# Kernel optimization log

Measured on AMD Instinct MI355X. Metric: run time of the kernel, lower is better.

The kernel has to match this reference:

```python
import jax, jax.numpy as jnp
import numpy as np

S = 100   # n_pred_samples
B = 64    # batch
DIMS = [784, 512, 512, 10]


def setup_inputs() -> dict:
    key = jax.random.key(0)
    ks = jax.random.split(key, 16)
    d = {}
    d["inputs"] = jax.random.normal(ks[0], (B, DIMS[0]), dtype=jnp.float32)
    d["task_id"] = 0
    # variational params: means ~ 0.1*N(0,1), logvars constant -6 (as in module init)
    d["wm0"] = jax.random.normal(ks[1], (DIMS[0], DIMS[1])) * 0.1
    d["wv0"] = jnp.full((DIMS[0], DIMS[1]), -6.0, jnp.float32)
    d["bm0"] = jnp.full((DIMS[1],), 0.1, jnp.float32)
    d["bv0"] = jnp.full((DIMS[1],), -6.0, jnp.float32)
    d["wm1"] = jax.random.normal(ks[2], (DIMS[1], DIMS[2])) * 0.1
    d["wv1"] = jnp.full((DIMS[1], DIMS[2]), -6.0, jnp.float32)
    d["bm1"] = jnp.full((DIMS[2],), 0.1, jnp.float32)
    d["bv1"] = jnp.full((DIMS[2],), -6.0, jnp.float32)
    d["wml"] = jax.random.normal(ks[3], (DIMS[2], DIMS[3])) * 0.1
    d["wvl"] = jnp.full((DIMS[2], DIMS[3]), -6.0, jnp.float32)
    d["bml"] = jnp.full((DIMS[3],), 0.1, jnp.float32)
    d["bvl"] = jnp.full((DIMS[3],), -6.0, jnp.float32)
    # reparameterization noise (passed explicitly for determinism)
    d["we0"] = jax.random.normal(ks[4], (S, DIMS[0], DIMS[1]), dtype=jnp.float32)
    d["be0"] = jax.random.normal(ks[5], (S, 1, DIMS[1]), dtype=jnp.float32)
    d["we1"] = jax.random.normal(ks[6], (S, DIMS[1], DIMS[2]), dtype=jnp.float32)
    d["be1"] = jax.random.normal(ks[7], (S, 1, DIMS[2]), dtype=jnp.float32)
    d["wel"] = jax.random.normal(ks[8], (S, DIMS[2], DIMS[3]), dtype=jnp.float32)
    d["bel"] = jax.random.normal(ks[9], (S, 1, DIMS[3]), dtype=jnp.float32)
    return d


def _sample(eps, logvar, mean):
    # reparameterization: eps * exp(0.5*logvar) + mean
    return eps * jnp.exp(0.5 * logvar) + mean


def reference(inputs, task_id, wm0, wv0, bm0, bv0, wm1, wv1, bm1, bv1,
              wml, wvl, bml, bvl, we0, be0, we1, be1, wel, bel):
    # activations: [S, B, D]
    act = jnp.broadcast_to(inputs[None], (S,) + inputs.shape)
    # hidden layer 0
    W0 = _sample(we0, wv0, wm0)          # [S, D0, D1]
    b0 = _sample(be0, bv0, bm0)          # [S, 1, D1]
    act = jax.nn.relu(jnp.einsum('sbi,sio->sbo', act, W0) + b0)
    # hidden layer 1
    W1 = _sample(we1, wv1, wm1)
    b1 = _sample(be1, bv1, bm1)
    act = jax.nn.relu(jnp.einsum('sbi,sio->sbo', act, W1) + b1)
    # last (task-specific) layer: original does broadcast-mul + sum over dim 2,
    # which is exactly a batched matmul — expressed here as an einsum
    Wl = _sample(wel, wvl, wml)          # [S, D2, O]
    bl = _sample(bel, bvl, bml)          # [S, 1, O]
    logits = jnp.einsum('sbh,sho->sbo', act, Wl) + bl   # [S, B, O]
    return logits
```

## Files before the change

### kernel.cpp

```cpp
#include <hip/hip_runtime.h>
#include <hip/hip_bf16.h>


typedef __bf16 bf16x8 __attribute__((ext_vector_type(8)));
typedef float f32x4 __attribute__((ext_vector_type(4)));

#define NSAMP 100
#define BATCH 64
#define D0 784
#define D1 512
#define D2 512
#define DOUT 10
#define K0PAD 800
#define RSB 40

__device__ __forceinline__ unsigned short f2bf(float f) {
    __bf16 b = (__bf16)f;
    return __builtin_bit_cast(unsigned short, b);
}
__device__ __forceinline__ float bf_hi(unsigned int u) {
    return __builtin_bit_cast(float, u & 0xffff0000u);
}
__device__ __forceinline__ float bf_lo(unsigned int u) {
    return __builtin_bit_cast(float, u << 16);
}

union FragU { uint4 q; bf16x8 v; };

#define XB_N   (BATCH * K0PAD)
#define PS0_N  (D0 * D1)
#define PS1_N  (D1 * D2)
#define SGL_N  (D2 * DOUT)
#define B0_N   (NSAMP * D1)
#define B1_N   (NSAMP * D2)
#define BL_N   (NSAMP * DOUT)
#define PREP_TOTAL (XB_N + PS0_N + PS1_N + SGL_N + B0_N + B1_N + BL_N)

__global__ __launch_bounds__(256) void prep(
    const float* __restrict__ inputs,
    const float* __restrict__ wv0, const float* __restrict__ wm0,
    const float* __restrict__ wv1, const float* __restrict__ wm1,
    const float* __restrict__ wvl,
    const float* __restrict__ be0, const float* __restrict__ bv0, const float* __restrict__ bm0,
    const float* __restrict__ be1, const float* __restrict__ bv1, const float* __restrict__ bm1,
    const float* __restrict__ bel, const float* __restrict__ bvl, const float* __restrict__ bml,
    unsigned short* __restrict__ Xb,
    unsigned int* __restrict__ psm0, unsigned int* __restrict__ psm1,
    float* __restrict__ sigmal,
    float* __restrict__ bias0, float* __restrict__ bias1, float* __restrict__ biasl)
{
    int i = blockIdx.x * 256 + threadIdx.x;
    if (i < XB_N) {
        int m = i / K0PAD, k = i % K0PAD;
        float v = (k < D0) ? inputs[m * D0 + k] : 0.f;
        Xb[i] = f2bf(v);
        return;
    }
    i -= XB_N;
    if (i < PS0_N) {
        unsigned int sg = f2bf(__expf(0.5f * wv0[i]));
        unsigned int mn = f2bf(wm0[i]);
        psm0[i] = (sg << 16) | mn;
        return;
    }
    i -= PS0_N;
    if (i < PS1_N) {
        unsigned int sg = f2bf(__expf(0.5f * wv1[i]));
        unsigned int mn = f2bf(wm1[i]);
        psm1[i] = (sg << 16) | mn;
        return;
    }
    i -= PS1_N;
    if (i < SGL_N) { sigmal[i] = __expf(0.5f * wvl[i]); return; }
    i -= SGL_N;
    if (i < B0_N) { int n = i % D1; bias0[i] = fmaf(be0[i], __expf(0.5f * bv0[n]), bm0[n]); return; }
    i -= B0_N;
    if (i < B1_N) { int n = i % D2; bias1[i] = fmaf(be1[i], __expf(0.5f * bv1[n]), bm1[n]); return; }
    i -= B1_N;
    if (i < BL_N) { int o = i % DOUT; biasl[i] = fmaf(bel[i], __expf(0.5f * bvl[o]), bml[o]); return; }
}

__global__ __launch_bounds__(64) void gemm_wave(
    const unsigned short* __restrict__ A, int lda, long aStride,
    const float* __restrict__ eps, long eStride,
    const unsigned int* __restrict__ psm,
    int KT, int Kvalid,
    const float* __restrict__ bias,
    void* __restrict__ outp, int outBf16)
{
    __shared__ unsigned short smB[32 * RSB];

    const int bx = blockIdx.x;
    const int s  = bx >> 4;
    const int n0 = (bx & 15) << 5;
    const int l  = threadIdx.x;
    const int fr = l & 15, quad = l >> 4;
    const int kg = l >> 3;
    const int ng = l & 7;

    const unsigned short* aP = A + (long)s * aStride + (long)fr * lda + quad * 8;
    const float* eB        = eps + (long)s * eStride + n0 + 4 * ng;
    const unsigned int* pB = psm + n0 + 4 * ng;

    f32x4 acc[4][2] = {};

    float4 ea0[4], ea1[4];
    uint4  pa0[4], pa1[4], aa0[4], aa1[4];

    auto loadAll = [&](int kt, float4* ea, uint4* pa, uint4* aa) {
        const int kb = kt * 32;
#pragma unroll
        for (int mi = 0; mi < 4; ++mi)
            aa[mi] = *reinterpret_cast<const uint4*>(aP + (long)(mi * 16) * lda + kb);
#pragma unroll
        for (int j = 0; j < 4; ++j) {
            const int row = kb + 4 * kg + j;
            const bool ok = row < Kvalid;
            const long off = (long)(ok ? row : 0) * 512;
            float4 e = *reinterpret_cast<const float4*>(eB + off);
            uint4  p = *reinterpret_cast<const uint4*>(pB + off);
            if (!ok) { e = float4{0.f, 0.f, 0.f, 0.f}; p = uint4{0u, 0u, 0u, 0u}; }
            ea[j] = e; pa[j] = p;
        }
    };

    auto stage = [&](const float4* ea, const uint4* pa) {
        float w[4][4];
#pragma unroll
        for (int j = 0; j < 4; ++j) {
            w[j][0] = fmaf(ea[j].x, bf_hi(pa[j].x), bf_lo(pa[j].x));
            w[j][1] = fmaf(ea[j].y, bf_hi(pa[j].y), bf_lo(pa[j].y));
            w[j][2] = fmaf(ea[j].z, bf_hi(pa[j].z), bf_lo(pa[j].z));
            w[j][3] = fmaf(ea[j].w, bf_hi(pa[j].w), bf_lo(pa[j].w));
        }
#pragma unroll
        for (int i = 0; i < 4; ++i) {
            uint2 d;
            d.x = (unsigned)f2bf(w[0][i]) | ((unsigned)f2bf(w[1][i]) << 16);
            d.y = (unsigned)f2bf(w[2][i]) | ((unsigned)f2bf(w[3][i]) << 16);
            *reinterpret_cast<uint2*>(&smB[(4 * ng + i) * RSB + 4 * kg]) = d;
        }
    };

    auto compute = [&](const uint4* aa) {
        FragU bf0, bf1;
        bf0.q = *reinterpret_cast<const uint4*>(&smB[fr * RSB + quad * 8]);
        bf1.q = *reinterpret_cast<const uint4*>(&smB[(16 + fr) * RSB + quad * 8]);
#pragma unroll
        for (int mi = 0; mi < 4; ++mi) {
            FragU af; af.q = aa[mi];
            acc[mi][0] = __builtin_amdgcn_mfma_f32_16x16x32_bf16(af.v, bf0.v, acc[mi][0], 0, 0, 0);
            acc[mi][1] = __builtin_amdgcn_mfma_f32_16x16x32_bf16(af.v, bf1.v, acc[mi][1], 0, 0, 0);
        }
    };

    loadAll(0, ea0, pa0, aa0);
    int kt = 0;
    for (; kt + 2 <= KT; kt += 2) {
        loadAll(kt + 1, ea1, pa1, aa1);
        stage(ea0, pa0);
        compute(aa0);
        if (kt + 2 < KT) loadAll(kt + 2, ea0, pa0, aa0);
        stage(ea1, pa1);
        compute(aa1);
    }
    if (kt < KT) { stage(ea0, pa0); compute(aa0); }

    const float bv0v = bias[(long)s * 512 + n0 + fr];
    const float bv1v = bias[(long)s * 512 + n0 + 16 + fr];
    const long outBase = (long)s * BATCH * 512;
#pragma unroll
    for (int mi = 0; mi < 4; ++mi) {
#pragma unroll
        for (int ni = 0; ni < 2; ++ni) {
            const float bv = ni ? bv1v : bv0v;
            const int col = n0 + ni * 16 + fr;
#pragma unroll
            for (int r = 0; r < 4; ++r) {
                const int row = mi * 16 + quad * 4 + r;
                float v = fmaxf(acc[mi][ni][r] + bv, 0.f);
                const long idx = outBase + (long)row * 512 + col;
                if (outBf16) ((unsigned short*)outp)[idx] = f2bf(v);
                else         ((float*)outp)[idx] = v;
            }
        }
    }
}

__global__ __launch_bounds__(320) void last_layer(
    const float* __restrict__ act2,
    const float* __restrict__ wel,
    const float* __restrict__ sigmal,
    const float* __restrict__ wml,
    const float* __restrict__ biasl,
    float* __restrict__ out)
{
    __shared__ float smW[D2 * DOUT];
    const int s = blockIdx.x;
    const int t = threadIdx.x;
    const float* we = wel + (long)s * D2 * DOUT;
    for (int i = t; i < D2 * DOUT; i += 320)
        smW[i] = fmaf(we[i], sigmal[i], wml[i]);
    __syncthreads();

    const int m  = t / 5;
    const int op = t % 5;
    const float* a = act2 + ((long)s * BATCH + m) * D2;
    float acc0 = 0.f, acc1 = 0.f;
#pragma unroll 4
    for (int k = 0; k < D2; k += 4) {
        float4 av = *reinterpret_cast<const float4*>(a + k);
        acc0 = fmaf(av.x, smW[(k + 0) * DOUT + op], acc0);
        acc0 = fmaf(av.y, smW[(k + 1) * DOUT + op], acc0);
        acc0 = fmaf(av.z, smW[(k + 2) * DOUT + op], acc0);
        acc0 = fmaf(av.w, smW[(k + 3) * DOUT + op], acc0);
        acc1 = fmaf(av.x, smW[(k + 0) * DOUT + op + 5], acc1);
        acc1 = fmaf(av.y, smW[(k + 1) * DOUT + op + 5], acc1);
        acc1 = fmaf(av.z, smW[(k + 2) * DOUT + op + 5], acc1);
        acc1 = fmaf(av.w, smW[(k + 3) * DOUT + op + 5], acc1);
    }
    const long ob = ((long)s * BATCH + m) * DOUT;
    out[ob + op]     = acc0 + biasl[s * DOUT + op];
    out[ob + op + 5] = acc1 + biasl[s * DOUT + op + 5];
}

extern "C" void kernel_launch(void* const* d_in, const int* in_sizes, int n_in,
                              void* d_out, int out_size, void* d_ws, size_t ws_size,
                              hipStream_t stream)
{
    const float* inputs = (const float*)d_in[0];
    const float* wm0 = (const float*)d_in[2];
    const float* wv0 = (const float*)d_in[3];
    const float* bm0 = (const float*)d_in[4];
    const float* bv0 = (const float*)d_in[5];
    const float* wm1 = (const float*)d_in[6];
    const float* wv1 = (const float*)d_in[7];
    const float* bm1 = (const float*)d_in[8];
    const float* bv1 = (const float*)d_in[9];
    const float* wml = (const float*)d_in[10];
    const float* wvl = (const float*)d_in[11];
    const float* bml = (const float*)d_in[12];
    const float* bvl = (const float*)d_in[13];
    const float* we0 = (const float*)d_in[14];
    const float* be0 = (const float*)d_in[15];
    const float* we1 = (const float*)d_in[16];
    const float* be1 = (const float*)d_in[17];
    const float* wel = (const float*)d_in[18];
    const float* bel = (const float*)d_in[19];

    char* w = (char*)d_ws;
    unsigned short* Xb  = (unsigned short*)w; w += (size_t)XB_N * 2;
    unsigned int* psm0  = (unsigned int*)w;   w += (size_t)PS0_N * 4;
    unsigned int* psm1  = (unsigned int*)w;   w += (size_t)PS1_N * 4;
    float* sigmal = (float*)w; w += (size_t)SGL_N * 4;
    float* bias0  = (float*)w; w += (size_t)B0_N * 4;
    float* bias1  = (float*)w; w += (size_t)B1_N * 4;
    float* biasl  = (float*)w; w += (size_t)BL_N * 4;
    unsigned short* act1 = (unsigned short*)w; w += (size_t)NSAMP * BATCH * D1 * 2;
    float* act2 = (float*)w; w += (size_t)NSAMP * BATCH * D2 * 4;

    prep<<<dim3((PREP_TOTAL + 255) / 256), 256, 0, stream>>>(
        inputs, wv0, wm0, wv1, wm1, wvl,
        be0, bv0, bm0, be1, bv1, bm1, bel, bvl, bml,
        Xb, psm0, psm1, sigmal, bias0, bias1, biasl);

    gemm_wave<<<dim3(NSAMP * 16), 64, 0, stream>>>(
        Xb, K0PAD, 0L, we0, (long)D0 * D1, psm0,
        K0PAD / 32, D0, bias0, (void*)act1, 1);

    gemm_wave<<<dim3(NSAMP * 16), 64, 0, stream>>>(
        act1, D1, (long)BATCH * D1, we1, (long)D1 * D2, psm1,
        D1 / 32, D1, bias1, (void*)act2, 0);

    last_layer<<<dim3(NSAMP), 320, 0, stream>>>(
        act2, wel, sigmal, wml, biasl, (float*)d_out);
}
```

Baseline: 407.3 us.

## Split weight sampling into a separate kernel writing MFMA-fragment-ordered bf16 weights

Weight sampling (eps*sigma+mean, converted to bf16) moves out of the GEMM into a new build_w kernel. That kernel writes the sampled weights straight into the per-lane B-fragment order that the MFMA instruction consumes, and each block reuses its loaded mean/sigma values across 4 samples. The GEMM then only streams pre-swizzled bf16 fragments and activations, with no shared-memory staging or barriers, over a 16-wide N tile per wave. The aim is to decouple the latency-bound elementwise sampling from the MFMA loop. The cost is an extra global write and re-read of all sampled weights (roughly half the size of the eps tensors) and a larger workspace.

```diff
diff --git a/kernel.cpp b/kernel.cpp
--- a/kernel.cpp
+++ b/kernel.cpp
@@ -12,7 +12,8 @@
 #define D2 512
 #define DOUT 10
 #define K0PAD 800
-#define RSB 40
+#define KT0 (K0PAD / 32)
+#define KT1 (D1 / 32)
 
 __device__ __forceinline__ unsigned short f2bf(float f) {
     __bf16 b = (__bf16)f;
@@ -80,109 +81,106 @@
     if (i < BL_N) { int o = i % DOUT; biasl[i] = fmaf(bel[i], __expf(0.5f * bvl[o]), bml[o]); return; }
 }
 
-__global__ __launch_bounds__(64) void gemm_wave(
-    const unsigned short* __restrict__ A, int lda, long aStride,
+__global__ __launch_bounds__(64) void build_w(
     const float* __restrict__ eps, long eStride,
     const unsigned int* __restrict__ psm,
-    int KT, int Kvalid,
+    uint4* __restrict__ Wb,
+    int KT, int Kvalid)
+{
+    const int bid = blockIdx.x;
+    const int kt  = bid % KT;
+    const int nb  = (bid / KT) & 31;
+    const int sg  = bid / (KT * 32);
+    const int l   = threadIdx.x;
+    const int fr  = l & 15, quad = l >> 4;
+    const int col   = nb * 16 + fr;
+    const int kbase = kt * 32 + quad * 8;
+
+    int rows[8];
+    unsigned int pv[8];
+#pragma unroll
+    for (int j = 0; j < 8; ++j) {
+        int r = kbase + j; if (r >= Kvalid) r = Kvalid - 1;
+        rows[j] = r;
+        pv[j] = psm[(long)r * 512 + col];
+    }
+#pragma unroll
+    for (int si = 0; si < 4; ++si) {
+        const int s = sg * 4 + si;
+        const float* eB = eps + (long)s * eStride + col;
+        float w[8];
+#pragma unroll
+        for (int j = 0; j < 8; ++j) {
+            float e = eB[(long)rows[j] * 512];
+            w[j] = fmaf(e, bf_hi(pv[j]), bf_lo(pv[j]));
+        }
+        uint4 o;
+        o.x = (unsigned)f2bf(w[0]) | ((unsigned)f2bf(w[1]) << 16);
+        o.y = (unsigned)f2bf(w[2]) | ((unsigned)f2bf(w[3]) << 16);
+        o.z = (unsigned)f2bf(w[4]) | ((unsigned)f2bf(w[5]) << 16);
+        o.w = (unsigned)f2bf(w[6]) | ((unsigned)f2bf(w[7]) << 16);
+        Wb[(((long)s * 32 + nb) * KT + kt) * 64 + l] = o;
+    }
+}
+
+__global__ __launch_bounds__(64) void gemm_pw(
+    const unsigned short* __restrict__ A, int lda, long aStride,
+    const uint4* __restrict__ Wb,
+    int KT,
     const float* __restrict__ bias,
     void* __restrict__ outp, int outBf16)
 {
-    __shared__ unsigned short smB[32 * RSB];
-
     const int bx = blockIdx.x;
-    const int s  = bx >> 4;
-    const int n0 = (bx & 15) << 5;
+    const int s  = bx >> 5;
+    const int nb = bx & 31;
     const int l  = threadIdx.x;
     const int fr = l & 15, quad = l >> 4;
-    const int kg = l >> 3;
-    const int ng = l & 7;
 
     const unsigned short* aP = A + (long)s * aStride + (long)fr * lda + quad * 8;
-    const float* eB        = eps + (long)s * eStride + n0 + 4 * ng;
-    const unsigned int* pB = psm + n0 + 4 * ng;
-
-    f32x4 acc[4][2] = {};
-
-    float4 ea0[4], ea1[4];
-    uint4  pa0[4], pa1[4], aa0[4], aa1[4];
-
-    auto loadAll = [&](int kt, float4* ea, uint4* pa, uint4* aa) {
+    const uint4* wP = Wb + ((long)s * 32 + nb) * KT * 64 + l;
+
+    f32x4 acc[4] = {};
+    uint4 wA, wB, aA[4], aB[4];
+
+    auto issue = [&](int kt, uint4& w, uint4* a) {
+        w = wP[(long)kt * 64];
         const int kb = kt * 32;
 #pragma unroll
         for (int mi = 0; mi < 4; ++mi)
-            aa[mi] = *reinterpret_cast<const uint4*>(aP + (long)(mi * 16) * lda + kb);
-#pragma unroll
-        for (int j = 0; j < 4; ++j) {
-            const int row = kb + 4 * kg + j;
-            const bool ok = row < Kvalid;
-            const long off = (long)(ok ? row : 0) * 512;
-            float4 e = *reinterpret_cast<const float4*>(eB + off);
-            uint4  p = *reinterpret_cast<const uint4*>(pB + off);
-            if (!ok) { e = float4{0.f, 0.f, 0.f, 0.f}; p = uint4{0u, 0u, 0u, 0u}; }
-            ea[j] = e; pa[j] = p;
+            a[mi] = *reinterpret_cast<const uint4*>(aP + (long)(mi * 16) * lda + kb);
+    };
+    auto comp = [&](const uint4& w, const uint4* a) {
+        FragU bf; bf.q = w;
+#pragma unroll
+        for (int mi = 0; mi < 4; ++mi) {
+            FragU af; af.q = a[mi];
+            acc[mi] = __builtin_amdgcn_mfma_f32_16x16x32_bf16(af.v, bf.v, acc[mi], 0, 0, 0);
         }
     };
 
-    auto stage = [&](const float4* ea, const uint4* pa) {
-        float w[4][4];
-#pragma unroll
-        for (int j = 0; j < 4; ++j) {
-            w[j][0] = fmaf(ea[j].x, bf_hi(pa[j].x), bf_lo(pa[j].x));
-            w[j][1] = fmaf(ea[j].y, bf_hi(pa[j].y), bf_lo(pa[j].y));
-            w[j][2] = fmaf(ea[j].z, bf_hi(pa[j].z), bf_lo(pa[j].z));
-            w[j][3] = fmaf(ea[j].w, bf_hi(pa[j].w), bf_lo(pa[j].w));
-        }
-#pragma unroll
-        for (int i = 0; i < 4; ++i) {
-            uint2 d;
-            d.x = (unsigned)f2bf(w[0][i]) | ((unsigned)f2bf(w[1][i]) << 16);
-            d.y = (unsigned)f2bf(w[2][i]) | ((unsigned)f2bf(w[3][i]) << 16);
-            *reinterpret_cast<uint2*>(&smB[(4 * ng + i) * RSB + 4 * kg]) = d;
-        }
-    };
-
-    auto compute = [&](const uint4* aa) {
-        FragU bf0, bf1;
-        bf0.q = *reinterpret_cast<const uint4*>(&smB[fr * RSB + quad * 8]);
-        bf1.q = *reinterpret_cast<const uint4*>(&smB[(16 + fr) * RSB + quad * 8]);
-#pragma unroll
-        for (int mi = 0; mi < 4; ++mi) {
-            FragU af; af.q = aa[mi];
-            acc[mi][0] = __builtin_amdgcn_mfma_f32_16x16x32_bf16(af.v, bf0.v, acc[mi][0], 0, 0, 0);
-            acc[mi][1] = __builtin_amdgcn_mfma_f32_16x16x32_bf16(af.v, bf1.v, acc[mi][1], 0, 0, 0);
-        }
-    };
-
-    loadAll(0, ea0, pa0, aa0);
+    issue(0, wA, aA);
     int kt = 0;
-    for (; kt + 2 <= KT; kt += 2) {
-        loadAll(kt + 1, ea1, pa1, aa1);
-        stage(ea0, pa0);
-        compute(aa0);
-        if (kt + 2 < KT) loadAll(kt + 2, ea0, pa0, aa0);
-        stage(ea1, pa1);
-        compute(aa1);
-    }
-    if (kt < KT) { stage(ea0, pa0); compute(aa0); }
-
-    const float bv0v = bias[(long)s * 512 + n0 + fr];
-    const float bv1v = bias[(long)s * 512 + n0 + 16 + fr];
-    const long outBase = (long)s * BATCH * 512;
+    while (kt < KT) {
+        if (kt + 1 < KT) issue(kt + 1, wB, aB);
+        comp(wA, aA);
+        ++kt;
+        if (kt >= KT) break;
+        if (kt + 1 < KT) issue(kt + 1, wA, aA);
+        comp(wB, aB);
+        ++kt;
+    }
+
+    const float bv = bias[(long)s * 512 + nb * 16 + fr];
+    const long outBase = (long)s * BATCH * 512 + nb * 16 + fr;
 #pragma unroll
     for (int mi = 0; mi < 4; ++mi) {
 #pragma unroll
-        for (int ni = 0; ni < 2; ++ni) {
-            const float bv = ni ? bv1v : bv0v;
-            const int col = n0 + ni * 16 + fr;
-#pragma unroll
-            for (int r = 0; r < 4; ++r) {
-                const int row = mi * 16 + quad * 4 + r;
-                float v = fmaxf(acc[mi][ni][r] + bv, 0.f);
-                const long idx = outBase + (long)row * 512 + col;
-                if (outBf16) ((unsigned short*)outp)[idx] = f2bf(v);
-                else         ((float*)outp)[idx] = v;
-            }
+        for (int r = 0; r < 4; ++r) {
+            const int row = mi * 16 + quad * 4 + r;
+            float v = fmaxf(acc[mi][r] + bv, 0.f);
+            const long idx = outBase + (long)row * 512;
+            if (outBf16) ((unsigned short*)outp)[idx] = f2bf(v);
+            else         ((float*)outp)[idx] = v;
         }
     }
 }
@@ -258,19 +256,24 @@
     float* biasl  = (float*)w; w += (size_t)BL_N * 4;
     unsigned short* act1 = (unsigned short*)w; w += (size_t)NSAMP * BATCH * D1 * 2;
     float* act2 = (float*)w; w += (size_t)NSAMP * BATCH * D2 * 4;
+    uint4* W0 = (uint4*)w; w += (size_t)NSAMP * 32 * KT0 * 64 * 16;
+    uint4* W1 = (uint4*)w; w += (size_t)NSAMP * 32 * KT1 * 64 * 16;
 
     prep<<<dim3((PREP_TOTAL + 255) / 256), 256, 0, stream>>>(
         inputs, wv0, wm0, wv1, wm1, wvl,
         be0, bv0, bm0, be1, bv1, bm1, bel, bvl, bml,
         Xb, psm0, psm1, sigmal, bias0, bias1, biasl);
 
-    gemm_wave<<<dim3(NSAMP * 16), 64, 0, stream>>>(
-        Xb, K0PAD, 0L, we0, (long)D0 * D1, psm0,
-        K0PAD / 32, D0, bias0, (void*)act1, 1);
-
-    gemm_wave<<<dim3(NSAMP * 16), 64, 0, stream>>>(
-        act1, D1, (long)BATCH * D1, we1, (long)D1 * D2, psm1,
-        D1 / 32, D1, bias1, (void*)act2, 0);
+    build_w<<<dim3((NSAMP / 4) * 32 * KT0), 64, 0, stream>>>(
+        we0, (long)D0 * D1, psm0, W0, KT0, D0);
+    build_w<<<dim3((NSAMP / 4) * 32 * KT1), 64, 0, stream>>>(
+        we1, (long)D1 * D2, psm1, W1, KT1, D1);
+
+    gemm_pw<<<dim3(NSAMP * 32), 64, 0, stream>>>(
+        Xb, K0PAD, 0L, W0, KT0, bias0, (void*)act1, 1);
+
+    gemm_pw<<<dim3(NSAMP * 32), 64, 0, stream>>>(
+        act1, D1, (long)BATCH * D1, W1, KT1, bias1, (void*)act2, 0);
 
     last_layer<<<dim3(NSAMP), 320, 0, stream>>>(
         act2, wel, sigmal, wml, biasl, (float*)d_out);
```

Result: slower. 449.6 us (+10.4%).
